# Optimization experiments

Hardware: AMD Instinct MI355X
Metric: run time of the kernel (lower is better)

## Reference

```python
import jax, jax.numpy as jnp
import numpy as np

N_HEAD = 16


def setup_inputs() -> dict:
    key = jax.random.key(0)
    ks = jax.random.split(key, 3)
    B, T, C = 4, 2048, 1024
    x = jax.random.normal(ks[0], (B, T, C), dtype=jnp.float32)
    w_attn = jax.random.normal(ks[1], (3 * C, C), dtype=jnp.float32) * (1.0 / np.sqrt(C))
    b_attn = jnp.zeros((3 * C,), dtype=jnp.float32)
    w_proj = jax.random.normal(ks[2], (C, C), dtype=jnp.float32) * (1.0 / np.sqrt(C))
    b_proj = jnp.zeros((C,), dtype=jnp.float32)
    return {"x": x, "w_attn": w_attn, "b_attn": b_attn, "w_proj": w_proj, "b_proj": b_proj}


def reference(x, w_attn, b_attn, w_proj, b_proj):
    B, T, C = x.shape
    H = N_HEAD
    D = C // H
    qkv = x @ w_attn.T + b_attn                      # [B, T, 3C]
    q, k, v = jnp.split(qkv, 3, axis=-1)
    # [B, T, C] -> [B, H, T, D]
    q = q.reshape(B, T, H, D).transpose(0, 2, 1, 3)
    k = k.reshape(B, T, H, D).transpose(0, 2, 1, 3)
    v = v.reshape(B, T, H, D).transpose(0, 2, 1, 3)
    scale = 1.0 / np.sqrt(D).astype(np.float32)
    att = jnp.einsum('bhqd,bhkd->bhqk', q, k) * scale  # [B, H, T, T]
    causal = jnp.tril(jnp.ones((T, T), dtype=bool))
    att = jnp.where(causal[None, None], att, -jnp.inf)
    att = jax.nn.softmax(att, axis=-1)
    y = jnp.einsum('bhqk,bhkd->bhqd', att, v)          # [B, H, T, D]
    y = y.transpose(0, 2, 1, 3).reshape(B, T, C)
    return y @ w_proj.T + b_proj
```

## Files before the change

### kernel.cpp

```cpp
#include <hip/hip_runtime.h>
#include <hip/hip_bf16.h>
#include <stdint.h>

typedef __attribute__((ext_vector_type(8))) short bf16x8;
typedef __attribute__((ext_vector_type(8))) unsigned short ushort8;
typedef __attribute__((ext_vector_type(4))) float f32x4;

#define MFMA16(a, b, c) __builtin_amdgcn_mfma_f32_16x16x32_bf16((a), (b), (c), 0, 0, 0)

__device__ __forceinline__ unsigned short f2bf(float f) {
  unsigned int u = __builtin_bit_cast(unsigned int, f);
  unsigned int r = (u + 0x7fffu + ((u >> 16) & 1u)) >> 16;
  return (unsigned short)r;
}

__device__ __forceinline__ void gload16(const unsigned short* g, unsigned short* lds_dst) {
  __builtin_amdgcn_global_load_lds(
      (const __attribute__((address_space(1))) unsigned int*)g,
      (__attribute__((address_space(3))) unsigned int*)lds_dst, 16, 0, 0);
}

__global__ void cvt_all(const float* __restrict__ x, const float* __restrict__ wa,
                        const float* __restrict__ wp, unsigned short* __restrict__ xb,
                        unsigned short* __restrict__ wab, unsigned short* __restrict__ wpb) {
  const int C0 = 1048576;
  const int C1 = 1441792;
  const int C2 = 1572864;
  int i = blockIdx.x * blockDim.x + threadIdx.x;
  const int stride = gridDim.x * blockDim.x;
  for (; i < C2; i += stride) {
    const float* src; unsigned short* dst; long e;
    if (i < C0)      { src = x;  dst = xb;  e = (long)i * 8; }
    else if (i < C1) { src = wa; dst = wab; e = (long)(i - C0) * 8; }
    else             { src = wp; dst = wpb; e = (long)(i - C1) * 8; }
    float4 v0 = *(const float4*)(src + e);
    float4 v1 = *(const float4*)(src + e + 4);
    ushort8 o;
    o[0] = f2bf(v0.x); o[1] = f2bf(v0.y); o[2] = f2bf(v0.z); o[3] = f2bf(v0.w);
    o[4] = f2bf(v1.x); o[5] = f2bf(v1.y); o[6] = f2bf(v1.z); o[7] = f2bf(v1.w);
    *(ushort8*)(dst + e) = o;
  }
}

template <int EPI, int NB>
__global__ __launch_bounds__(512, 2)
void gemm_bt(const unsigned short* __restrict__ A,
             const unsigned short* __restrict__ Bt,
             const float* __restrict__ bias,
             int M, int N, int K,
             unsigned short* __restrict__ q_out,
             unsigned short* __restrict__ k_out,
             unsigned short* __restrict__ vt_out,
             float* __restrict__ f_out) {
  constexpr int BNT = NB * 64;
  alignas(16) __shared__ unsigned short Alds[2][2][128 * 64];
  alignas(16) __shared__ unsigned short Blds[2][BNT * 64];
  const int t = threadIdx.x, w = t >> 6, l = t & 63;
  const int bm = blockIdx.x, bn = blockIdx.y;
  const int wm = w >> 2, wn = w & 3;
  const int lo = l & 15, hi = l >> 4, swk = lo & 7;

  f32x4 acc[8][NB];
  const f32x4 zero = {0.f, 0.f, 0.f, 0.f};
#pragma unroll
  for (int i = 0; i < 8; ++i)
#pragma unroll
    for (int j = 0; j < NB; ++j) acc[i][j] = zero;

  const int sr = t >> 3;
  const int gsrcE = ((t & 7) ^ (sr & 7)) * 8;
  const unsigned short* Asrc = A + (long)(bm * 256 + sr) * K + gsrcE;
  const unsigned short* Bsrc = Bt + (long)(bn * BNT + sr) * K + gsrcE;

#define STAGE_AH(sb, qh, koff) do {                                    \
    unsigned short* d_ = &Alds[sb][qh][w * 512];                       \
    const unsigned short* s_ = Asrc + (long)(qh) * 64 * K + (koff);    \
    gload16(s_, d_); gload16(s_ + 128L * K, d_ + 4096); } while (0)
#define STAGE_B(sb, koff) do {                                         \
    _Pragma("unroll")                                                  \
    for (int c_ = 0; c_ < NB; ++c_)                                    \
      gload16(Bsrc + (long)c_ * 64 * K + (koff),                       \
              &Blds[sb][c_ * 4096 + w * 512]); } while (0)

  STAGE_AH(0, 0, 0);
  STAGE_B(0, 0);
  STAGE_AH(0, 1, 0);
  asm volatile("s_waitcnt vmcnt(2)" ::: "memory");
  __builtin_amdgcn_sched_barrier(0);
  __builtin_amdgcn_s_barrier();

  const int lrA = (wm * 64 + lo) * 64;
  const int lrB = (wn * (NB * 16) + lo) * 64;
  const int gk0 = ((hi) ^ swk) * 8;
  const int gk1 = ((4 + hi) ^ swk) * 8;

  bf16x8 af[4][2], blo[2][2], bhi[2];

  for (int kt = 0; kt < 16; ++kt) {
    const int c = kt & 1, nb = c ^ 1;
    const bool st = (kt < 15);
    const int koff = (kt + 1) * 64;
    const unsigned short* A0 = Alds[c][0];
    const unsigned short* A1 = Alds[c][1];
    const unsigned short* Bs = Blds[c];

#pragma unroll
    for (int ii = 0; ii < 4; ++ii) {
      af[ii][0] = *(const bf16x8*)&A0[lrA + ii * 1024 + gk0];
      af[ii][1] = *(const bf16x8*)&A0[lrA + ii * 1024 + gk1];
    }
#pragma unroll
    for (int jj = 0; jj < NB - 1; ++jj) {
      blo[jj][0] = *(const bf16x8*)&Bs[lrB + jj * 1024 + gk0];
      blo[jj][1] = *(const bf16x8*)&Bs[lrB + jj * 1024 + gk1];
    }
    if (st) STAGE_AH(nb, 0, koff);
    __builtin_amdgcn_s_barrier();
    asm volatile("s_waitcnt lgkmcnt(0)" ::: "memory");
    __builtin_amdgcn_sched_barrier(0);
    __builtin_amdgcn_s_setprio(1);
#pragma unroll
    for (int ii = 0; ii < 4; ++ii)
#pragma unroll
      for (int jj = 0; jj < NB - 1; ++jj) {
        acc[ii][jj] = MFMA16(af[ii][0], blo[jj][0], acc[ii][jj]);
        acc[ii][jj] = MFMA16(af[ii][1], blo[jj][1], acc[ii][jj]);
      }
    __builtin_amdgcn_s_setprio(0);
    __builtin_amdgcn_s_barrier();

    bhi[0] = *(const bf16x8*)&Bs[lrB + (NB - 1) * 1024 + gk0];
    bhi[1] = *(const bf16x8*)&Bs[lrB + (NB - 1) * 1024 + gk1];
    if (st) STAGE_B(nb, koff);
    __builtin_amdgcn_s_barrier();
    asm volatile("s_waitcnt lgkmcnt(0)" ::: "memory");
    __builtin_amdgcn_sched_barrier(0);
    __builtin_amdgcn_s_setprio(1);
#pragma unroll
    for (int ii = 0; ii < 4; ++ii) {
      acc[ii][NB - 1] = MFMA16(af[ii][0], bhi[0], acc[ii][NB - 1]);
      acc[ii][NB - 1] = MFMA16(af[ii][1], bhi[1], acc[ii][NB - 1]);
    }
    __builtin_amdgcn_s_setprio(0);
    if (st) {
      if constexpr (NB == 3) { asm volatile("s_waitcnt vmcnt(5)" ::: "memory"); }
      else                   { asm volatile("s_waitcnt vmcnt(4)" ::: "memory"); }
    } else {
      asm volatile("s_waitcnt vmcnt(0)" ::: "memory");
    }
    __builtin_amdgcn_sched_barrier(0);
    __builtin_amdgcn_s_barrier();

#pragma unroll
    for (int ii = 0; ii < 4; ++ii) {
      af[ii][0] = *(const bf16x8*)&A1[lrA + ii * 1024 + gk0];
      af[ii][1] = *(const bf16x8*)&A1[lrA + ii * 1024 + gk1];
    }
    if (st) STAGE_AH(nb, 1, koff);
    __builtin_amdgcn_s_barrier();
    asm volatile("s_waitcnt lgkmcnt(0)" ::: "memory");
    __builtin_amdgcn_sched_barrier(0);
    __builtin_amdgcn_s_setprio(1);
#pragma unroll
    for (int ii = 0; ii < 4; ++ii) {
      acc[4 + ii][NB - 1] = MFMA16(af[ii][0], bhi[0], acc[4 + ii][NB - 1]);
      acc[4 + ii][NB - 1] = MFMA16(af[ii][1], bhi[1], acc[4 + ii][NB - 1]);
    }
    __builtin_amdgcn_s_setprio(0);
    __builtin_amdgcn_s_barrier();

    __builtin_amdgcn_s_setprio(1);
#pragma unroll
    for (int ii = 0; ii < 4; ++ii)
#pragma unroll
      for (int jj = 0; jj < NB - 1; ++jj) {
        acc[4 + ii][jj] = MFMA16(af[ii][0], blo[jj][0], acc[4 + ii][jj]);
        acc[4 + ii][jj] = MFMA16(af[ii][1], blo[jj][1], acc[4 + ii][jj]);
      }
    __builtin_amdgcn_s_setprio(0);
    if (st) {
      asm volatile("s_waitcnt vmcnt(2)" ::: "memory");
      __builtin_amdgcn_sched_barrier(0);
    }
    __builtin_amdgcn_s_barrier();
  }
#undef STAGE_AH
#undef STAGE_B

#pragma unroll
  for (int i = 0; i < 8; ++i) {
#pragma unroll
    for (int j = 0; j < NB; ++j) {
#pragma unroll
      for (int r = 0; r < 4; ++r) {
        int row = bm * 256 + wm * 128 + i * 16 + hi * 4 + r;
        int col = bn * BNT + wn * (NB * 16) + j * 16 + lo;
        float v = acc[i][j][r] + bias[col];
        if (EPI == 0) {
          int b = row >> 11, tt = row & 2047;
          int seg = col >> 10, cc = col & 1023;
          int h = cc >> 6, d = cc & 63;
          long bh = (long)(b * 16 + h);
          if (seg == 0)      q_out[(bh * 2048 + tt) * 64 + d] = f2bf(v * 0.1803368801111f);
          else if (seg == 1) k_out[(bh * 2048 + tt) * 64 + d] = f2bf(v);
          else               vt_out[(bh * 64 + d) * 2048 + tt] = f2bf(v);
        } else {
          f_out[(long)row * N + col] = v;
        }
      }
    }
  }
}

__global__ __launch_bounds__(512, 4)
void attn_kernel(const unsigned short* __restrict__ Q,
                 const unsigned short* __restrict__ K,
                 const unsigned short* __restrict__ Vt,
                 unsigned short* __restrict__ Y) {
  alignas(16) __shared__ unsigned short Kbuf[2][64 * 64];
  alignas(16) __shared__ unsigned short Vbuf[2][64 * 64];
  alignas(16) __shared__ unsigned short pbuf[8][16 * 64];
  const int t = threadIdx.x, w = t >> 6, l = t & 63;
  const int lo = l & 15, hi = l >> 4;
  const int bh = blockIdx.x;
  const int p = blockIdx.y;
  const int b = bh >> 4, h = bh & 15;
  const int sA = p, sB = 15 - p;
  const int nA = 2 * p + 2;
  const int nTot = 34;
  const unsigned short* Qp = Q + (long)bh * 2048 * 64;
  const unsigned short* Kp = K + (long)bh * 2048 * 64;
  const unsigned short* Vp = Vt + (long)bh * 64 * 2048;
  unsigned short* pw = pbuf[w];

  const short one_bf = (short)0x3F80;
  const bf16x8 ones = {one_bf, one_bf, one_bf, one_bf, one_bf, one_bf, one_bf, one_bf};
  const f32x4 zero = {0.f, 0.f, 0.f, 0.f};

  const int qbA = sA * 128 + w * 16;
  const int qbB = sB * 128 + w * 16;

  bf16x8 qf0, qf1;
  f32x4 lsum;
  f32x4 oacc[4];

  qf0 = *(const bf16x8*)&Qp[(qbA + lo) * 64 + hi * 8];
  qf1 = *(const bf16x8*)&Qp[(qbA + lo) * 64 + 32 + hi * 8];
  lsum = zero;
#pragma unroll
  for (int dg = 0; dg < 4; ++dg) oacc[dg] = zero;

  const int srow = t >> 3;
  const int scw = ((t & 7) ^ (srow & 7)) * 8;
  const int sw = lo & 7;

#define STAGE(kvoff, bufidx)                                          \
  do {                                                                \
    unsigned short* KB_ = Kbuf[bufidx] + w * 512;                     \
    unsigned short* VB_ = Vbuf[bufidx] + w * 512;                     \
    gload16(Kp + (long)((kvoff) + srow) * 64 + scw, KB_);             \
    gload16(Vp + (long)srow * 2048 + (kvoff) + scw, VB_);             \
  } while (0)

  STAGE(0, 0);
  __syncthreads();

  for (int g = 0; g < nTot; ++g) {
    const bool inA = (g < nA);
    const int kvb = (inA ? g : g - nA) * 64;
    const int cur = g & 1;
    if (g + 1 < nTot) {
      const int jn = (g + 1 < nA) ? g + 1 : g + 1 - nA;
      STAGE(jn * 64, cur ^ 1);
    }
    const int qbase = inA ? qbA : qbB;
    if (kvb <= qbase + 15) {
      const unsigned short* KB = Kbuf[cur];
      const unsigned short* VB = Vbuf[cur];
      f32x4 s[4];
#pragma unroll
      for (int cg = 0; cg < 4; ++cg) s[cg] = zero;
      __builtin_amdgcn_s_setprio(1);
#pragma unroll
      for (int cg = 0; cg < 4; ++cg) {
        bf16x8 k0 = *(const bf16x8*)&KB[(cg * 16 + lo) * 64 + ((hi) ^ sw) * 8];
        bf16x8 k1 = *(const bf16x8*)&KB[(cg * 16 + lo) * 64 + ((4 + hi) ^ sw) * 8];
        s[cg] = MFMA16(k0, qf0, s[cg]);
        s[cg] = MFMA16(k1, qf1, s[cg]);
      }
      __builtin_amdgcn_s_setprio(0);
      if (kvb + 63 > qbase) {
        const int limit = qbase + lo - kvb;
#pragma unroll
        for (int cg = 0; cg < 4; ++cg)
#pragma unroll
          for (int r = 0; r < 4; ++r)
            if (cg * 16 + hi * 4 + r > limit) s[cg][r] = -__builtin_inff();
      }
#pragma unroll
      for (int cg = 0; cg < 4; ++cg) {
        float p0 = exp2f(s[cg][0]);
        float p1 = exp2f(s[cg][1]);
        float p2 = exp2f(s[cg][2]);
        float p3 = exp2f(s[cg][3]);
        unsigned int u0, u1;
        asm("v_cvt_pk_bf16_f32 %0, %1, %2" : "=v"(u0) : "v"(p0), "v"(p1));
        asm("v_cvt_pk_bf16_f32 %0, %1, %2" : "=v"(u1) : "v"(p2), "v"(p3));
        const int gg = (cg * 2 + (hi >> 1)) ^ sw;
        uint2 val; val.x = u0; val.y = u1;
        *(uint2*)&pw[lo * 64 + gg * 8 + (hi & 1) * 4] = val;
      }
      asm volatile("s_waitcnt lgkmcnt(0)" ::: "memory");
      bf16x8 pa0 = *(const bf16x8*)&pw[lo * 64 + ((hi) ^ sw) * 8];
      bf16x8 pa1 = *(const bf16x8*)&pw[lo * 64 + ((4 + hi) ^ sw) * 8];
      __builtin_amdgcn_s_setprio(1);
      lsum = MFMA16(pa0, ones, lsum);
      lsum = MFMA16(pa1, ones, lsum);
#pragma unroll
      for (int dg = 0; dg < 4; ++dg) {
        bf16x8 vv0 = *(const bf16x8*)&VB[(dg * 16 + lo) * 64 + ((hi) ^ sw) * 8];
        bf16x8 vv1 = *(const bf16x8*)&VB[(dg * 16 + lo) * 64 + ((4 + hi) ^ sw) * 8];
        oacc[dg] = MFMA16(pa0, vv0, oacc[dg]);
        oacc[dg] = MFMA16(pa1, vv1, oacc[dg]);
      }
      __builtin_amdgcn_s_setprio(0);
    }
    if (g == nA - 1) {
#pragma unroll
      for (int r = 0; r < 4; ++r) {
        float inv = 1.0f / lsum[r];
        int rowg = qbA + hi * 4 + r;
        long base = ((long)b * 2048 + rowg) * 1024 + h * 64;
#pragma unroll
        for (int dg = 0; dg < 4; ++dg)
          Y[base + dg * 16 + lo] = f2bf(oacc[dg][r] * inv);
      }
      qf0 = *(const bf16x8*)&Qp[(qbB + lo) * 64 + hi * 8];
      qf1 = *(const bf16x8*)&Qp[(qbB + lo) * 64 + 32 + hi * 8];
      lsum = zero;
#pragma unroll
      for (int dg = 0; dg < 4; ++dg) oacc[dg] = zero;
    }
    __syncthreads();
  }

#pragma unroll
  for (int r = 0; r < 4; ++r) {
    float inv = 1.0f / lsum[r];
    int rowg = qbB + hi * 4 + r;
    long base = ((long)b * 2048 + rowg) * 1024 + h * 64;
#pragma unroll
    for (int dg = 0; dg < 4; ++dg)
      Y[base + dg * 16 + lo] = f2bf(oacc[dg][r] * inv);
  }
#undef STAGE
}

extern "C" void kernel_launch(void* const* d_in, const int* in_sizes, int n_in,
                              void* d_out, int out_size, void* d_ws, size_t ws_size,
                              hipStream_t stream) {
  const float* x      = (const float*)d_in[0];
  const float* w_attn = (const float*)d_in[1];
  const float* b_attn = (const float*)d_in[2];
  const float* w_proj = (const float*)d_in[3];
  const float* b_proj = (const float*)d_in[4];
  float* out = (float*)d_out;

  const long NX = 8192L * 1024;
  const long NWA = 3072L * 1024;
  const long NWP = 1024L * 1024;
  const long NQ = 64L * 2048 * 64;

  char* ws = (char*)d_ws;
  unsigned short* xb  = (unsigned short*)ws; ws += NX * 2;
  unsigned short* wab = (unsigned short*)ws; ws += NWA * 2;
  unsigned short* wpb = (unsigned short*)ws; ws += NWP * 2;
  unsigned short* qb  = (unsigned short*)ws; ws += NQ * 2;
  unsigned short* kb  = (unsigned short*)ws; ws += NQ * 2;
  unsigned short* vtb = (unsigned short*)ws; ws += NQ * 2;
  unsigned short* yb  = (unsigned short*)ws; ws += NX * 2;

  cvt_all<<<2048, 256, 0, stream>>>(x, w_attn, w_proj, xb, wab, wpb);

  dim3 g1(32, 16);
  gemm_bt<0, 3><<<g1, 512, 0, stream>>>(xb, wab, b_attn, 8192, 3072, 1024,
                                        qb, kb, vtb, nullptr);
  dim3 ga(64, 8);
  attn_kernel<<<ga, 512, 0, stream>>>(qb, kb, vtb, yb);
  dim3 g2(32, 8);
  gemm_bt<1, 2><<<g2, 512, 0, stream>>>(yb, wpb, b_proj, 8192, 1024, 1024,
                                        nullptr, nullptr, nullptr, out);
}
```

Measured before the change: 177.0 us.

## Replace paired causal query tiles with one tile per block, heaviest first

The attention kernel no longer pairs a light and a heavy 128-row query tile in one block to balance causal work. Each block now handles a single query tile, the grid doubles to 64x16, and blocks are ordered so the longest tiles are launched first. Launch bounds rise from 4 to 6 blocks per CU, which limits registers per thread to allow more resident blocks. This removes the mid-loop output write and Q reload, but blocks now vary widely in length and the tighter register limit may cause spills.

```diff
diff --git a/kernel.cpp b/kernel.cpp
--- a/kernel.cpp
+++ b/kernel.cpp
@@ -212,7 +212,7 @@
   }
 }
 
-__global__ __launch_bounds__(512, 4)
+__global__ __launch_bounds__(512, 6)
 void attn_kernel(const unsigned short* __restrict__ Q,
                  const unsigned short* __restrict__ K,
                  const unsigned short* __restrict__ Vt,
@@ -223,11 +223,9 @@
   const int t = threadIdx.x, w = t >> 6, l = t & 63;
   const int lo = l & 15, hi = l >> 4;
   const int bh = blockIdx.x;
-  const int p = blockIdx.y;
+  const int s = 15 - blockIdx.y;
   const int b = bh >> 4, h = bh & 15;
-  const int sA = p, sB = 15 - p;
-  const int nA = 2 * p + 2;
-  const int nTot = 34;
+  const int nTot = 2 * s + 2;
   const unsigned short* Qp = Q + (long)bh * 2048 * 64;
   const unsigned short* Kp = K + (long)bh * 2048 * 64;
   const unsigned short* Vp = Vt + (long)bh * 64 * 2048;
@@ -237,15 +235,14 @@
   const bf16x8 ones = {one_bf, one_bf, one_bf, one_bf, one_bf, one_bf, one_bf, one_bf};
   const f32x4 zero = {0.f, 0.f, 0.f, 0.f};
 
-  const int qbA = sA * 128 + w * 16;
-  const int qbB = sB * 128 + w * 16;
+  const int qb = s * 128 + w * 16;
 
   bf16x8 qf0, qf1;
   f32x4 lsum;
   f32x4 oacc[4];
 
-  qf0 = *(const bf16x8*)&Qp[(qbA + lo) * 64 + hi * 8];
-  qf1 = *(const bf16x8*)&Qp[(qbA + lo) * 64 + 32 + hi * 8];
+  qf0 = *(const bf16x8*)&Qp[(qb + lo) * 64 + hi * 8];
+  qf1 = *(const bf16x8*)&Qp[(qb + lo) * 64 + 32 + hi * 8];
   lsum = zero;
 #pragma unroll
   for (int dg = 0; dg < 4; ++dg) oacc[dg] = zero;
@@ -266,43 +263,40 @@
   __syncthreads();
 
   for (int g = 0; g < nTot; ++g) {
-    const bool inA = (g < nA);
-    const int kvb = (inA ? g : g - nA) * 64;
+    const int kvb = g * 64;
     const int cur = g & 1;
     if (g + 1 < nTot) {
-      const int jn = (g + 1 < nA) ? g + 1 : g + 1 - nA;
-      STAGE(jn * 64, cur ^ 1);
-    }
-    const int qbase = inA ? qbA : qbB;
-    if (kvb <= qbase + 15) {
+      STAGE((g + 1) * 64, cur ^ 1);
+    }
+    if (kvb <= qb + 15) {
       const unsigned short* KB = Kbuf[cur];
       const unsigned short* VB = Vbuf[cur];
-      f32x4 s[4];
-#pragma unroll
-      for (int cg = 0; cg < 4; ++cg) s[cg] = zero;
+      f32x4 sc[4];
+#pragma unroll
+      for (int cg = 0; cg < 4; ++cg) sc[cg] = zero;
       __builtin_amdgcn_s_setprio(1);
 #pragma unroll
       for (int cg = 0; cg < 4; ++cg) {
         bf16x8 k0 = *(const bf16x8*)&KB[(cg * 16 + lo) * 64 + ((hi) ^ sw) * 8];
         bf16x8 k1 = *(const bf16x8*)&KB[(cg * 16 + lo) * 64 + ((4 + hi) ^ sw) * 8];
-        s[cg] = MFMA16(k0, qf0, s[cg]);
-        s[cg] = MFMA16(k1, qf1, s[cg]);
+        sc[cg] = MFMA16(k0, qf0, sc[cg]);
+        sc[cg] = MFMA16(k1, qf1, sc[cg]);
       }
       __builtin_amdgcn_s_setprio(0);
-      if (kvb + 63 > qbase) {
-        const int limit = qbase + lo - kvb;
+      if (kvb + 63 > qb) {
+        const int limit = qb + lo - kvb;
 #pragma unroll
         for (int cg = 0; cg < 4; ++cg)
 #pragma unroll
           for (int r = 0; r < 4; ++r)
-            if (cg * 16 + hi * 4 + r > limit) s[cg][r] = -__builtin_inff();
+            if (cg * 16 + hi * 4 + r > limit) sc[cg][r] = -__builtin_inff();
       }
 #pragma unroll
       for (int cg = 0; cg < 4; ++cg) {
-        float p0 = exp2f(s[cg][0]);
-        float p1 = exp2f(s[cg][1]);
-        float p2 = exp2f(s[cg][2]);
-        float p3 = exp2f(s[cg][3]);
+        float p0 = exp2f(sc[cg][0]);
+        float p1 = exp2f(sc[cg][1]);
+        float p2 = exp2f(sc[cg][2]);
+        float p3 = exp2f(sc[cg][3]);
         unsigned int u0, u1;
         asm("v_cvt_pk_bf16_f32 %0, %1, %2" : "=v"(u0) : "v"(p0), "v"(p1));
         asm("v_cvt_pk_bf16_f32 %0, %1, %2" : "=v"(u1) : "v"(p2), "v"(p3));
@@ -325,29 +319,13 @@
       }
       __builtin_amdgcn_s_setprio(0);
     }
-    if (g == nA - 1) {
-#pragma unroll
-      for (int r = 0; r < 4; ++r) {
-        float inv = 1.0f / lsum[r];
-        int rowg = qbA + hi * 4 + r;
-        long base = ((long)b * 2048 + rowg) * 1024 + h * 64;
-#pragma unroll
-        for (int dg = 0; dg < 4; ++dg)
-          Y[base + dg * 16 + lo] = f2bf(oacc[dg][r] * inv);
-      }
-      qf0 = *(const bf16x8*)&Qp[(qbB + lo) * 64 + hi * 8];
-      qf1 = *(const bf16x8*)&Qp[(qbB + lo) * 64 + 32 + hi * 8];
-      lsum = zero;
-#pragma unroll
-      for (int dg = 0; dg < 4; ++dg) oacc[dg] = zero;
-    }
     __syncthreads();
   }
 
 #pragma unroll
   for (int r = 0; r < 4; ++r) {
     float inv = 1.0f / lsum[r];
-    int rowg = qbB + hi * 4 + r;
+    int rowg = qb + hi * 4 + r;
     long base = ((long)b * 2048 + rowg) * 1024 + h * 64;
 #pragma unroll
     for (int dg = 0; dg < 4; ++dg)
@@ -385,7 +363,7 @@
   dim3 g1(32, 16);
   gemm_bt<0, 3><<<g1, 512, 0, stream>>>(xb, wab, b_attn, 8192, 3072, 1024,
                                         qb, kb, vtb, nullptr);
-  dim3 ga(64, 8);
+  dim3 ga(64, 16);
   attn_kernel<<<ga, 512, 0, stream>>>(qb, kb, vtb, yb);
   dim3 g2(32, 8);
   gemm_bt<1, 2><<<g2, 512, 0, stream>>>(yb, wpb, b_proj, 8192, 1024, 1024,
```

Measured after the change: 172.9 us. -2.3%, faster.
